# Kernel tuning notes

Measured on AMD Instinct MI355X. Metric: run time of the kernel, lower is better.

## Reference

```python
import jax, jax.numpy as jnp
import numpy as np

N, E, D, H, L = 10000, 80000, 1024, 8, 2
C = D // H          # 128 per-head channels
NEG = 0.2           # GATv2 default negative_slope


def setup_inputs() -> dict:
    k = jax.random.split(jax.random.key(0), 16)
    s = 0.02
    return {
        "x": jax.random.normal(k[0], (N, D), jnp.float32),
        "edge_index": jax.random.randint(k[1], (2, E), 0, N),
        "edge_attr": jax.random.randint(k[2], (E,), 0, 3),
        "node_types": jax.random.randint(k[3], (N,), 0, 5),
        "node_type_emb": s * jax.random.normal(k[4], (5, D), jnp.float32),
        "edge_type_emb": s * jax.random.normal(k[5], (3, D), jnp.float32),
        "Wl": s * jax.random.normal(k[6], (L, D, D), jnp.float32),
        "bl": jnp.zeros((L, D), jnp.float32),
        "Wr": s * jax.random.normal(k[7], (L, D, D), jnp.float32),
        "br": jnp.zeros((L, D), jnp.float32),
        "We": s * jax.random.normal(k[8], (L, D, D), jnp.float32),
        "att": s * jax.random.normal(k[9], (L, H, C), jnp.float32),
        "conv_bias": jnp.zeros((L, D), jnp.float32),
        "out_W": s * jax.random.normal(k[10], (D, D), jnp.float32),
        "out_b": jnp.zeros((D,), jnp.float32),
    }


def _gatv2(h, src, dst, ee, Wl, bl, Wr, br, We, att, b):
    """PyG GATv2Conv: concat=True, add_self_loops=True (fill_value='mean')."""
    n = h.shape[0]
    xl = (h @ Wl + bl).reshape(n, H, C)   # source transform (lin_l)
    xr = (h @ Wr + br).reshape(n, H, C)   # target transform (lin_r)
    # self loops: edge_attr of a loop = mean of raw incoming edge feats
    cnt = jax.ops.segment_sum(jnp.ones(src.shape, jnp.float32), dst, num_segments=n)
    loop_attr = jax.ops.segment_sum(ee, dst, num_segments=n) / jnp.maximum(cnt, 1.0)[:, None]
    loops = jnp.arange(n)
    s2 = jnp.concatenate([src, loops])
    d2 = jnp.concatenate([dst, loops])
    ea = jnp.concatenate([ee, loop_attr], axis=0)          # [E+N, D]
    ep = (ea @ We).reshape(-1, H, C)                        # lin_edge (no bias)
    e = jax.nn.leaky_relu(xl[s2] + xr[d2] + ep, NEG)        # [E+N, H, C]
    logit = jnp.einsum('ehc,hc->eh', e, att)                # attention logits
    # segment softmax over destination nodes (every node has a self loop)
    m = jax.ops.segment_max(logit, d2, num_segments=n)
    a = jnp.exp(logit - m[d2])
    alpha = a / jax.ops.segment_sum(a, d2, num_segments=n)[d2]
    out = jax.ops.segment_sum(alpha[:, :, None] * xl[s2], d2, num_segments=n)
    return out.reshape(n, D) + b


def reference(x, edge_index, edge_attr, node_types, node_type_emb, edge_type_emb,
              Wl, bl, Wr, br, We, att, conv_bias, out_W, out_b):
    h = x + node_type_emb[node_types]
    ee = edge_type_emb[edge_attr]
    src, dst = edge_index[0], edge_index[1]
    for i in range(L):  # num_layers = 2
        h = h + jax.nn.relu(_gatv2(h, src, dst, ee, Wl[i], bl[i], Wr[i], br[i],
                                   We[i], att[i], conv_bias[i]))
    return h @ out_W + out_b
```

## Files before the change

### kernel.cpp

```cpp
#include <hip/hip_runtime.h>
#include <hip/hip_bf16.h>
#include <stdint.h>

typedef __bf16 bf16_t;
typedef bf16_t bf16x8 __attribute__((ext_vector_type(8)));
typedef bf16_t bf16x4 __attribute__((ext_vector_type(4)));
typedef float f32x4 __attribute__((ext_vector_type(4)));

#define NN 10000
#define EE 80000
#define DD 1024
#define LL 2
#define MPAD 10112
#define NEGS 0.2f

#define GLOAD_LDS16(g, l) \
    __builtin_amdgcn_global_load_lds((__attribute__((address_space(1))) void*)(void*)(g), \
                                     (__attribute__((address_space(3))) void*)(l), 16, 0, 0)

__global__ __launch_bounds__(256)
void preamble(const float* __restrict__ Wl, const float* __restrict__ Wr,
              const float* __restrict__ outW, bf16_t* __restrict__ WT,
              bf16_t* __restrict__ OWT,
              const float* __restrict__ x, const int* __restrict__ ntypes,
              const float* __restrict__ nte, bf16_t* __restrict__ hbuf,
              const float* __restrict__ bl, const float* __restrict__ br,
              const float* __restrict__ outb, float* __restrict__ biasb,
              float* __restrict__ M3L, int* __restrict__ deg3)
{
    __shared__ float tile[64][65];
    int b = blockIdx.x;
    int tid = threadIdx.x;
    if (b < 1280) {
        int z = b >> 8, rem = b & 255;
        int bx = rem & 15, by = rem >> 4;
        const float* src;
        bf16_t* dstp;
        switch (z) {
            case 0: src = Wl;                       dstp = WT;                        break;
            case 1: src = Wr;                       dstp = WT + (size_t)1024*1024;    break;
            case 2: src = Wl + (size_t)1024*1024;   dstp = WT + (size_t)2*1024*1024;  break;
            case 3: src = Wr + (size_t)1024*1024;   dstp = WT + (size_t)3*1024*1024;  break;
            default: src = outW;                    dstp = OWT;                       break;
        }
        int tx = tid & 15, ty = tid >> 4;
#pragma unroll
        for (int p = 0; p < 4; ++p) {
            int r = ty + p*16;
            f32x4 rv = *(const f32x4*)(src + (size_t)(by*64 + r)*1024 + bx*64 + tx*4);
#pragma unroll
            for (int j = 0; j < 4; ++j) tile[r][tx*4 + j] = rv[j];
        }
        __syncthreads();
        int v = tid & 7, u0 = tid >> 3;
#pragma unroll
        for (int p = 0; p < 2; ++p) {
            int u = u0 + p*32;
            bf16x8 ov;
#pragma unroll
            for (int j = 0; j < 8; ++j) ov[j] = (bf16_t)tile[v*8 + j][u];
            *(bf16x8*)(dstp + (size_t)(bx*64 + u)*1024 + by*64 + v*8) = ov;
        }
    } else if (b < 6336) {
        size_t idx = ((size_t)(b - 1280)*256 + tid) * 8;
        if (idx >= (size_t)MPAD*1024) return;
        int n = (int)(idx >> 10);
        int c = (int)(idx & 1023);
        bf16x8 outv;
        if (n < NN) {
            const float* xp = x + (size_t)n*1024 + c;
            int t = ntypes[n];
            const float* ep = nte + (size_t)t*1024 + c;
            f32x4 xa = *(const f32x4*)(xp);
            f32x4 xb = *(const f32x4*)(xp + 4);
            f32x4 ea = *(const f32x4*)(ep);
            f32x4 eb = *(const f32x4*)(ep + 4);
#pragma unroll
            for (int j = 0; j < 4; ++j) {
                outv[j]     = (bf16_t)(xa[j] + ea[j]);
                outv[4 + j] = (bf16_t)(xb[j] + eb[j]);
            }
        } else {
#pragma unroll
            for (int j = 0; j < 8; ++j) outv[j] = (bf16_t)0.f;
        }
        *(bf16x8*)(hbuf + idx) = outv;
    } else if (b < 6356) {
        int i = (b - 6336)*256 + tid;
        if (i < 4096) {
            int l = i >> 11, j = i & 2047;
            biasb[i] = (j < 1024) ? bl[l*1024 + j] : br[l*1024 + j - 1024];
        } else if (i < 5120) {
            biasb[i] = outb[i - 4096];
        }
    } else if (b < 6380) {
        int i = (b - 6356)*256 + tid;
        if (i < LL*3072) M3L[i] = 0.f;
    } else {
        int i = (b - 6380)*256 + tid;
        if (i < 3*NN) deg3[i] = 0;
    }
}

__global__ __launch_bounds__(256)
void aux_k(const float* __restrict__ ete, const float* __restrict__ We,
           float* __restrict__ M3L,
           const int* __restrict__ dsts, const int* __restrict__ etype,
           int* __restrict__ deg3)
{
    int b = blockIdx.x;
    if (b < 512) {
        int l   = b >> 8;
        int bid = b & 255;
        const float* WeL = We + (size_t)l*1024*1024;
        float* M3 = M3L + l*3072;
        int j  = (bid & 3) * 256 + threadIdx.x;
        int k0 = (bid >> 2) * 16;
        float a0 = 0.f, a1 = 0.f, a2 = 0.f;
#pragma unroll
        for (int kk = 0; kk < 16; ++kk) {
            int k = k0 + kk;
            float w = WeL[(size_t)k*1024 + j];
            a0 += ete[k]        * w;
            a1 += ete[1024 + k] * w;
            a2 += ete[2048 + k] * w;
        }
        atomicAdd(&M3[j],        a0);
        atomicAdd(&M3[1024 + j], a1);
        atomicAdd(&M3[2048 + j], a2);
    } else {
        int e = (b - 512)*256 + threadIdx.x;
        if (e < EE) atomicAdd(&deg3[dsts[e]*3 + etype[e]], 1);
    }
}

__global__ __launch_bounds__(1024)
void scan_csr(const int* __restrict__ deg3, int* __restrict__ rp3, int* __restrict__ cursor3)
{
    __shared__ int tot[1024];
    int t = threadIdx.x;
    int base = t * 30;
    int v[30];
    int run = 0;
#pragma unroll
    for (int j = 0; j < 30; ++j) {
        int i = base + j;
        int d = (i < 3*NN) ? deg3[i] : 0;
        run += d;
        v[j] = run;
    }
    tot[t] = run;
    __syncthreads();
    for (int d = 1; d < 1024; d <<= 1) {
        int xv = (t >= d) ? tot[t - d] : 0;
        __syncthreads();
        tot[t] += xv;
        __syncthreads();
    }
    int ex = (t == 0) ? 0 : tot[t - 1];
#pragma unroll
    for (int j = 0; j < 30; ++j) {
        int i = base + j;
        if (i < 3*NN) {
            int incl = ex + v[j];
            rp3[i + 1] = incl;
            if (i + 1 < 3*NN) cursor3[i + 1] = incl;
        }
    }
    if (t == 0) { rp3[0] = 0; cursor3[0] = 0; }
}

__global__ void fill_csr(const int* __restrict__ srcs, const int* __restrict__ dsts,
                         const int* __restrict__ etype, int* __restrict__ cursor3,
                         int* __restrict__ sorted_src)
{
    int e = blockIdx.x*256 + threadIdx.x;
    if (e < EE) {
        int d = dsts[e];
        int t = etype[e];
        int pos = atomicAdd(&cursor3[d*3 + t], 1);
        sorted_src[pos] = srcs[e];
    }
}

template <typename OT>
__global__ __launch_bounds__(256)
void gemm_bt(const bf16_t* __restrict__ A, const bf16_t* __restrict__ BT,
             const float* __restrict__ bias, OT* __restrict__ Cmat,
             int K, int Ntot, int storeM, int mtiles, int ntiles)
{
    __shared__ __align__(16) bf16_t As[128*64];
    __shared__ __align__(16) bf16_t Bs[128*64];
    const int tid  = threadIdx.x;
    const int wave = tid >> 6;
    const int lane = tid & 63;

    const int GROUP_M = 8;
    const int nwg = gridDim.x;
    const int cpx = nwg >> 3;
    const int bidx = blockIdx.x;
    int pid = (bidx & 7) * cpx + (bidx >> 3);
    int in_group = GROUP_M * ntiles;
    int gid = pid / in_group;
    int first_m = gid * GROUP_M;
    int gsz = mtiles - first_m; if (gsz > GROUP_M) gsz = GROUP_M;
    int local = pid % in_group;
    const int m0 = (first_m + (local % gsz)) * 128;
    const int n0 = (local / gsz) * 128;

    const int wm = (wave & 1) * 64;
    const int wn = (wave >> 1) * 64;
    const int quad = lane >> 4;
    const int l16  = lane & 15;

    const int srow = lane >> 3;
    const int gcol = ((lane & 7) ^ srow) * 8;

    f32x4 acc[4][4];
    f32x4 zero = {0.f, 0.f, 0.f, 0.f};
#pragma unroll
    for (int i = 0; i < 4; ++i)
#pragma unroll
        for (int j = 0; j < 4; ++j) acc[i][j] = zero;

    const bf16_t* aBase = A  + (size_t)(m0 + wave*8 + srow) * K + gcol;
    const bf16_t* bBase = BT + (size_t)(n0 + wave*8 + srow) * K + gcol;
    bf16_t* asDst = As + wave*512;
    bf16_t* bsDst = Bs + wave*512;

    for (int k0 = 0; k0 < K; k0 += 64) {
#pragma unroll
        for (int j = 0; j < 4; ++j)
            GLOAD_LDS16(aBase + (size_t)(j*32)*K + k0, asDst + j*2048);
#pragma unroll
        for (int j = 0; j < 4; ++j)
            GLOAD_LDS16(bBase + (size_t)(j*32)*K + k0, bsDst + j*2048);
        __syncthreads();
#pragma unroll
        for (int kk = 0; kk < 2; ++kk) {
            bf16x8 af[4], bfr[4];
#pragma unroll
            for (int mi = 0; mi < 4; ++mi) {
                int row = wm + mi*16 + l16;
                int ch  = ((kk*4 + quad) ^ (row & 7)) * 8;
                af[mi] = *(const bf16x8*)(As + row*64 + ch);
            }
#pragma unroll
            for (int ni = 0; ni < 4; ++ni) {
                int row = wn + ni*16 + l16;
                int ch  = ((kk*4 + quad) ^ (row & 7)) * 8;
                bfr[ni] = *(const bf16x8*)(Bs + row*64 + ch);
            }
#pragma unroll
            for (int mi = 0; mi < 4; ++mi)
#pragma unroll
                for (int ni = 0; ni < 4; ++ni)
                    acc[mi][ni] = __builtin_amdgcn_mfma_f32_16x16x32_bf16(af[mi], bfr[ni], acc[mi][ni], 0, 0, 0);
        }
        __syncthreads();
    }

#pragma unroll
    for (int mi = 0; mi < 4; ++mi) {
#pragma unroll
        for (int ni = 0; ni < 4; ++ni) {
            int col = n0 + wn + ni*16 + l16;
            float bv = bias[col];
#pragma unroll
            for (int r = 0; r < 4; ++r) {
                int row = m0 + wm + mi*16 + quad*4 + r;
                if (row < storeM)
                    Cmat[(size_t)row * Ntot + col] = (OT)(acc[mi][ni][r] + bv);
            }
        }
    }
}

__global__ __launch_bounds__(256)
void fused_edge(const int* __restrict__ rp3, const int* __restrict__ ssrc,
                const bf16_t* __restrict__ XLXR,
                const float* __restrict__ M3, const float* __restrict__ attv,
                const float* __restrict__ cbias, bf16_t* __restrict__ hbuf)
{
    int node = blockIdx.x*2 + (threadIdx.x >> 7);
    int q = threadIdx.x & 127;
    int c8 = q * 8;

    int b   = __builtin_amdgcn_readfirstlane(rp3[3*node]);
    int t1g = __builtin_amdgcn_readfirstlane(rp3[3*node + 1]);
    int t2g = __builtin_amdgcn_readfirstlane(rp3[3*node + 2]);
    int en  = __builtin_amdgcn_readfirstlane(rp3[3*node + 3]);

    bf16x8 xlv = *(const bf16x8*)(XLXR + (size_t)node*2048 + c8);
    bf16x8 xrv = *(const bf16x8*)(XLXR + (size_t)node*2048 + 1024 + c8);
    float xr[8], at[8], q0[8], q1[8], q2[8];
#pragma unroll
    for (int j = 0; j < 8; ++j) xr[j] = (float)xrv[j];
    f32x4 a_lo = *(const f32x4*)(attv + c8);
    f32x4 a_hi = *(const f32x4*)(attv + c8 + 4);
#pragma unroll
    for (int j = 0; j < 4; ++j) { at[j] = a_lo[j]; at[4+j] = a_hi[j]; }
#pragma unroll
    for (int j = 0; j < 8; ++j) {
        q0[j] = xr[j] + M3[c8 + j];
        q1[j] = xr[j] + M3[1024 + c8 + j];
        q2[j] = xr[j] + M3[2048 + c8 + j];
    }

    float acc[8] = {0.f, 0.f, 0.f, 0.f, 0.f, 0.f, 0.f, 0.f};
    float den = 0.f;

    auto body = [&](int i, const float (&p)[8]) {
        int s = ssrc[i];
        bf16x8 xs = *(const bf16x8*)(XLXR + (size_t)s*2048 + c8);
        float x[8];
        float part = 0.f;
#pragma unroll
        for (int j = 0; j < 8; ++j) {
            x[j] = (float)xs[j];
            float v = x[j] + p[j];
            v = fmaxf(v, NEGS * v);
            part += v * at[j];
        }
        part += __shfl_xor(part, 1);
        part += __shfl_xor(part, 2);
        part += __shfl_xor(part, 4);
        part += __shfl_xor(part, 8);
        part = fminf(fmaxf(part, -60.f), 60.f);
        float pe = __expf(part);
        den += pe;
#pragma unroll
        for (int j = 0; j < 8; ++j) acc[j] += pe * x[j];
    };

#pragma unroll 2
    for (int i = b; i < t1g; ++i)   body(i, q0);
#pragma unroll 2
    for (int i = t1g; i < t2g; ++i) body(i, q1);
#pragma unroll 2
    for (int i = t2g; i < en; ++i)  body(i, q2);

    float cnt0 = (float)(t1g - b);
    float cnt1 = (float)(t2g - t1g);
    float cnt2 = (float)(en - t2g);
    float degf = cnt0 + cnt1 + cnt2;
    float inv = 1.f / fmaxf(degf, 1.f);
    float w0 = cnt0 * inv, w1 = cnt1 * inv, w2 = cnt2 * inv;
    float sw = w0 + w1 + w2;
    float sx[8];
    float sp = 0.f;
#pragma unroll
    for (int j = 0; j < 8; ++j) {
        sx[j] = (float)xlv[j];
        float u = sx[j] + xr[j]*(1.f - sw) + w0*q0[j] + w1*q1[j] + w2*q2[j];
        u = fmaxf(u, NEGS * u);
        sp += u * at[j];
    }
    sp += __shfl_xor(sp, 1);
    sp += __shfl_xor(sp, 2);
    sp += __shfl_xor(sp, 4);
    sp += __shfl_xor(sp, 8);
    sp = fminf(fmaxf(sp, -60.f), 60.f);
    float ps = __expf(sp);
    den += ps;
#pragma unroll
    for (int j = 0; j < 8; ++j) acc[j] += ps * sx[j];

    float invd = 1.f / den;
    bf16x8 hv = *(const bf16x8*)(hbuf + (size_t)node*1024 + c8);
    bf16x8 outv;
#pragma unroll
    for (int j = 0; j < 8; ++j)
        outv[j] = (bf16_t)((float)hv[j] + fmaxf(acc[j]*invd + cbias[c8 + j], 0.f));
    *(bf16x8*)(hbuf + (size_t)node*1024 + c8) = outv;
}

extern "C" void kernel_launch(void* const* d_in, const int* in_sizes, int n_in,
                              void* d_out, int out_size, void* d_ws, size_t ws_size,
                              hipStream_t stream)
{
    (void)in_sizes; (void)n_in; (void)out_size; (void)ws_size;
    const float* x     = (const float*)d_in[0];
    const int*   eidx  = (const int*)d_in[1];
    const int*   etype = (const int*)d_in[2];
    const int*   ntyp  = (const int*)d_in[3];
    const float* nte   = (const float*)d_in[4];
    const float* ete   = (const float*)d_in[5];
    const float* Wl    = (const float*)d_in[6];
    const float* bl    = (const float*)d_in[7];
    const float* Wr    = (const float*)d_in[8];
    const float* br    = (const float*)d_in[9];
    const float* We    = (const float*)d_in[10];
    const float* attw  = (const float*)d_in[11];
    const float* cbias = (const float*)d_in[12];
    const float* outW  = (const float*)d_in[13];
    const float* outb  = (const float*)d_in[14];
    const int* srcs = eidx;
    const int* dsts = eidx + EE;

    char* wsp = (char*)d_ws;
    size_t off = 0;
    auto carve = [&](size_t bytes) -> void* {
        void* pp = wsp + off;
        off += (bytes + 255) & ~(size_t)255;
        return pp;
    };
    bf16_t* hbuf  = (bf16_t*)carve((size_t)MPAD*1024*2);
    bf16_t* XLXR  = (bf16_t*)carve((size_t)MPAD*2048*2);
    bf16_t* WT    = (bf16_t*)carve((size_t)LL*2048*1024*2);
    bf16_t* OWT   = (bf16_t*)carve((size_t)1024*1024*2);
    float*  M3L   = (float*)carve((size_t)LL*3072*4);
    float*  biasb = (float*)carve(5120*4);
    int* deg3    = (int*)carve((size_t)3*NN*4);
    int* rp3     = (int*)carve((size_t)(3*NN+1)*4);
    int* cursor3 = (int*)carve((size_t)3*NN*4);
    int* ssrc    = (int*)carve((size_t)EE*4);

    preamble<<<6498, 256, 0, stream>>>(Wl, Wr, outW, WT, OWT,
                                       x, ntyp, nte, hbuf,
                                       bl, br, outb, biasb, M3L, deg3);
    aux_k<<<512 + (EE + 255)/256, 256, 0, stream>>>(ete, We, M3L, dsts, etype, deg3);
    scan_csr<<<1, 1024, 0, stream>>>(deg3, rp3, cursor3);
    fill_csr<<<(EE + 255)/256, 256, 0, stream>>>(srcs, dsts, etype, cursor3, ssrc);

    for (int l = 0; l < LL; ++l) {
        gemm_bt<bf16_t><<<79*16, 256, 0, stream>>>(hbuf, WT + (size_t)l*2048*1024,
                                                   biasb + l*2048, XLXR,
                                                   1024, 2048, MPAD, 79, 16);
        fused_edge<<<NN/2, 256, 0, stream>>>(rp3, ssrc, XLXR, M3L + l*3072, attw + l*1024,
                                             cbias + l*1024, hbuf);
    }

    gemm_bt<float><<<79*8, 256, 0, stream>>>(hbuf, OWT, biasb + 4096, (float*)d_out,
                                             1024, 1024, NN, 79, 8);
}
```

Before: 419.5 us.

## Merge aux and fill_csr kernels into preamble and first GEMM launches

Folds the We-projection and degree-count work from aux_k into the preamble kernel, replacing its zeroing blocks with hipMemsetAsync. The CSR fill is appended as extra blocks of the first layer's GEMM launch, so it runs alongside the GEMM instead of as its own launch. The goal is fewer kernel launches and less serialization between small kernels. The catch is that the atomics in preamble now rely on memsets ordered before it in the stream, and the fill blocks share GPU resources with the GEMM tiles.

```diff
diff --git a/kernel.cpp b/kernel.cpp
--- a/kernel.cpp
+++ b/kernel.cpp
@@ -13,6 +13,8 @@
 #define LL 2
 #define MPAD 10112
 #define NEGS 0.2f
+#define GEMM0_GRID 1264
+#define FILL_BLKS 313
 
 #define GLOAD_LDS16(g, l) \
     __builtin_amdgcn_global_load_lds((__attribute__((address_space(1))) void*)(void*)(g), \
@@ -26,7 +28,10 @@
               const float* __restrict__ nte, bf16_t* __restrict__ hbuf,
               const float* __restrict__ bl, const float* __restrict__ br,
               const float* __restrict__ outb, float* __restrict__ biasb,
-              float* __restrict__ M3L, int* __restrict__ deg3)
+              const float* __restrict__ ete, const float* __restrict__ We,
+              float* __restrict__ M3L,
+              const int* __restrict__ dsts, const int* __restrict__ etype,
+              int* __restrict__ deg3)
 {
     __shared__ float tile[64][65];
     int b = blockIdx.x;
@@ -93,28 +98,13 @@
         } else if (i < 5120) {
             biasb[i] = outb[i - 4096];
         }
-    } else if (b < 6380) {
-        int i = (b - 6356)*256 + tid;
-        if (i < LL*3072) M3L[i] = 0.f;
-    } else {
-        int i = (b - 6380)*256 + tid;
-        if (i < 3*NN) deg3[i] = 0;
-    }
-}
-
-__global__ __launch_bounds__(256)
-void aux_k(const float* __restrict__ ete, const float* __restrict__ We,
-           float* __restrict__ M3L,
-           const int* __restrict__ dsts, const int* __restrict__ etype,
-           int* __restrict__ deg3)
-{
-    int b = blockIdx.x;
-    if (b < 512) {
-        int l   = b >> 8;
-        int bid = b & 255;
+    } else if (b < 6868) {
+        int idx = b - 6356;
+        int l   = idx >> 8;
+        int bid = idx & 255;
         const float* WeL = We + (size_t)l*1024*1024;
         float* M3 = M3L + l*3072;
-        int j  = (bid & 3) * 256 + threadIdx.x;
+        int j  = (bid & 3) * 256 + tid;
         int k0 = (bid >> 2) * 16;
         float a0 = 0.f, a1 = 0.f, a2 = 0.f;
 #pragma unroll
@@ -129,7 +119,7 @@
         atomicAdd(&M3[1024 + j], a1);
         atomicAdd(&M3[2048 + j], a2);
     } else {
-        int e = (b - 512)*256 + threadIdx.x;
+        int e = (b - 6868)*256 + tid;
         if (e < EE) atomicAdd(&deg3[dsts[e]*3 + etype[e]], 1);
     }
 }
@@ -170,24 +160,11 @@
     if (t == 0) { rp3[0] = 0; cursor3[0] = 0; }
 }
 
-__global__ void fill_csr(const int* __restrict__ srcs, const int* __restrict__ dsts,
-                         const int* __restrict__ etype, int* __restrict__ cursor3,
-                         int* __restrict__ sorted_src)
-{
-    int e = blockIdx.x*256 + threadIdx.x;
-    if (e < EE) {
-        int d = dsts[e];
-        int t = etype[e];
-        int pos = atomicAdd(&cursor3[d*3 + t], 1);
-        sorted_src[pos] = srcs[e];
-    }
-}
-
 template <typename OT>
-__global__ __launch_bounds__(256)
-void gemm_bt(const bf16_t* __restrict__ A, const bf16_t* __restrict__ BT,
-             const float* __restrict__ bias, OT* __restrict__ Cmat,
-             int K, int Ntot, int storeM, int mtiles, int ntiles)
+__device__ __forceinline__
+void gemm_core(const bf16_t* __restrict__ A, const bf16_t* __restrict__ BT,
+               const float* __restrict__ bias, OT* __restrict__ Cmat,
+               int K, int Ntot, int storeM, int mtiles, int ntiles, int pid)
 {
     __shared__ __align__(16) bf16_t As[128*64];
     __shared__ __align__(16) bf16_t Bs[128*64];
@@ -196,10 +173,6 @@
     const int lane = tid & 63;
 
     const int GROUP_M = 8;
-    const int nwg = gridDim.x;
-    const int cpx = nwg >> 3;
-    const int bidx = blockIdx.x;
-    int pid = (bidx & 7) * cpx + (bidx >> 3);
     int in_group = GROUP_M * ntiles;
     int gid = pid / in_group;
     int first_m = gid * GROUP_M;
@@ -274,6 +247,38 @@
             }
         }
     }
+}
+
+template <typename OT>
+__global__ __launch_bounds__(256)
+void gemm_bt(const bf16_t* __restrict__ A, const bf16_t* __restrict__ BT,
+             const float* __restrict__ bias, OT* __restrict__ Cmat,
+             int K, int Ntot, int storeM, int mtiles, int ntiles)
+{
+    const int cpx = gridDim.x >> 3;
+    int pid = ((int)blockIdx.x & 7) * cpx + ((int)blockIdx.x >> 3);
+    gemm_core<OT>(A, BT, bias, Cmat, K, Ntot, storeM, mtiles, ntiles, pid);
+}
+
+__global__ __launch_bounds__(256)
+void gemm0_fill(const bf16_t* __restrict__ A, const bf16_t* __restrict__ BT,
+                const float* __restrict__ bias, bf16_t* __restrict__ Cmat,
+                const int* __restrict__ srcs, const int* __restrict__ dsts,
+                const int* __restrict__ etype, int* __restrict__ cursor3,
+                int* __restrict__ ssrc)
+{
+    if (blockIdx.x >= GEMM0_GRID) {
+        int e = ((int)blockIdx.x - GEMM0_GRID)*256 + (int)threadIdx.x;
+        if (e < EE) {
+            int d = dsts[e];
+            int t = etype[e];
+            int pos = atomicAdd(&cursor3[d*3 + t], 1);
+            ssrc[pos] = srcs[e];
+        }
+        return;
+    }
+    int pid = ((int)blockIdx.x & 7) * (GEMM0_GRID >> 3) + ((int)blockIdx.x >> 3);
+    gemm_core<bf16_t>(A, BT, bias, Cmat, 1024, 2048, MPAD, 79, 16, pid);
 }
 
 __global__ __launch_bounds__(256)
@@ -416,20 +421,24 @@
     int* cursor3 = (int*)carve((size_t)3*NN*4);
     int* ssrc    = (int*)carve((size_t)EE*4);
 
-    preamble<<<6498, 256, 0, stream>>>(Wl, Wr, outW, WT, OWT,
+    hipMemsetAsync(deg3, 0, (size_t)3*NN*4, stream);
+    hipMemsetAsync(M3L, 0, (size_t)LL*3072*4, stream);
+    preamble<<<7181, 256, 0, stream>>>(Wl, Wr, outW, WT, OWT,
                                        x, ntyp, nte, hbuf,
-                                       bl, br, outb, biasb, M3L, deg3);
-    aux_k<<<512 + (EE + 255)/256, 256, 0, stream>>>(ete, We, M3L, dsts, etype, deg3);
+                                       bl, br, outb, biasb,
+                                       ete, We, M3L,
+                                       dsts, etype, deg3);
     scan_csr<<<1, 1024, 0, stream>>>(deg3, rp3, cursor3);
-    fill_csr<<<(EE + 255)/256, 256, 0, stream>>>(srcs, dsts, etype, cursor3, ssrc);
-
-    for (int l = 0; l < LL; ++l) {
-        gemm_bt<bf16_t><<<79*16, 256, 0, stream>>>(hbuf, WT + (size_t)l*2048*1024,
-                                                   biasb + l*2048, XLXR,
-                                                   1024, 2048, MPAD, 79, 16);
-        fused_edge<<<NN/2, 256, 0, stream>>>(rp3, ssrc, XLXR, M3L + l*3072, attw + l*1024,
-                                             cbias + l*1024, hbuf);
-    }
+
+    gemm0_fill<<<GEMM0_GRID + FILL_BLKS, 256, 0, stream>>>(hbuf, WT, biasb, XLXR,
+                                                           srcs, dsts, etype, cursor3, ssrc);
+    fused_edge<<<NN/2, 256, 0, stream>>>(rp3, ssrc, XLXR, M3L, attw, cbias, hbuf);
+
+    gemm_bt<bf16_t><<<79*16, 256, 0, stream>>>(hbuf, WT + (size_t)2048*1024,
+                                               biasb + 2048, XLXR,
+                                               1024, 2048, MPAD, 79, 16);
+    fused_edge<<<NN/2, 256, 0, stream>>>(rp3, ssrc, XLXR, M3L + 3072, attw + 1024,
+                                         cbias + 1024, hbuf);
 
     gemm_bt<float><<<79*8, 256, 0, stream>>>(hbuf, OWT, biasb + 4096, (float*)d_out,
                                              1024, 1024, NN, 79, 8);
```

Result: faster. 409.6 us (-2.3%).
